# Optimization experiments

Measured on AMD Instinct MI355X. Metric: run time of the kernel, lower is better.

## Reference

```python
import jax, jax.numpy as jnp
import numpy as np

N_LAYERS = 2
D_CONV = 4
D_MODEL = 768
D_INNER = 1536
D_STATE = 16
D_DELTA = 48
B = 2
L = 1024
EPS = 1e-5


def setup_inputs() -> dict:
    key = jax.random.key(0)
    ks = jax.random.split(key, 8)
    s = 0.02
    x = jax.random.normal(ks[0], (B, L, D_MODEL), jnp.float32)
    in_proj_w = jax.random.normal(ks[1], (N_LAYERS, 2 * D_INNER, D_MODEL), jnp.float32) * s
    conv_w = jax.random.normal(ks[2], (N_LAYERS, D_INNER, 1, D_CONV), jnp.float32) * s
    conv_b = jnp.zeros((N_LAYERS, D_INNER), jnp.float32)
    xproj_w = jax.random.normal(ks[3], (N_LAYERS, D_DELTA + 2 * D_STATE, D_INNER), jnp.float32) * s
    dt_w = jax.random.normal(ks[4], (N_LAYERS, D_INNER, D_DELTA), jnp.float32) * s
    dt_b = jax.random.normal(ks[5], (N_LAYERS, D_INNER), jnp.float32) * s
    A_log = jnp.tile(jnp.log(jnp.arange(1, D_STATE + 1, dtype=jnp.float32)), (N_LAYERS, D_INNER, 1))
    D = jnp.ones((N_LAYERS, D_INNER), jnp.float32)
    out_proj_w = jax.random.normal(ks[6], (N_LAYERS, D_MODEL, D_INNER), jnp.float32) * s
    norm_w = jnp.ones((N_LAYERS, D_MODEL), jnp.float32)
    return dict(x=x, in_proj_w=in_proj_w, conv_w=conv_w, conv_b=conv_b,
                xproj_w=xproj_w, dt_w=dt_w, dt_b=dt_b, A_log=A_log, D=D,
                out_proj_w=out_proj_w, norm_w=norm_w)


def rms_norm(x, w):
    return w * x * jax.lax.rsqrt(jnp.mean(x * x, axis=-1, keepdims=True) + EPS)


def causal_depthwise_conv(x, w, b):
    # x: [B, L, D_INNER], w: [D_INNER, 1, K], b: [D_INNER]
    xc = x.transpose(0, 2, 1)  # [B, D, L]
    y = jax.lax.conv_general_dilated(
        xc, w, window_strides=(1,), padding=[(D_CONV - 1, 0)],
        dimension_numbers=("NCH", "OIH", "NCH"), feature_group_count=D_INNER)
    y = y + b[None, :, None]
    return y.transpose(0, 2, 1)  # [B, L, D]


def ssm(x, A_log, D, xproj_w, dt_w, dt_b):
    # x: [B, L, D_INNER]
    A = -jnp.exp(A_log)  # [D, N]
    dbc = jnp.einsum('bld,ed->ble', x, xproj_w)
    delta, Bc, C = jnp.split(dbc, [D_DELTA, D_DELTA + D_STATE], axis=-1)
    delta = jax.nn.softplus(jnp.einsum('blr,dr->bld', delta, dt_w) + dt_b)  # [B, L, D]
    dA = jnp.exp(delta[..., None] * A)                          # [B, L, D, N]
    dBx = delta[..., None] * Bc[:, :, None, :] * x[..., None]   # [B, L, D, N]

    def step(h, inp):
        dA_t, dBx_t, C_t = inp
        h = dA_t * h + dBx_t                      # [B, D, N]
        y = jnp.einsum('bdn,bn->bd', h, C_t)      # [B, D]
        return h, y

    h0 = jnp.zeros((x.shape[0], D_INNER, D_STATE), x.dtype)
    _, ys = jax.lax.scan(step, h0, (dA.transpose(1, 0, 2, 3),
                                    dBx.transpose(1, 0, 2, 3),
                                    C.transpose(1, 0, 2)))
    y = ys.transpose(1, 0, 2)  # [B, L, D]
    return y + D * x


def mamba_block(x, in_w, cw, cb, xp_w, dtw, dtb, Alog, Dp, out_w):
    xz = jnp.einsum('blm,em->ble', x, in_w)           # [B, L, 2*D_INNER]
    xi, z = jnp.split(xz, 2, axis=-1)
    xi = jax.nn.silu(causal_depthwise_conv(xi, cw, cb))
    y = ssm(xi, Alog, Dp, xp_w, dtw, dtb)
    out = y * jax.nn.silu(z)
    return jnp.einsum('bld,md->blm', out, out_w)


def reference(x, in_proj_w, conv_w, conv_b, xproj_w, dt_w, dt_b, A_log, D, out_proj_w, norm_w):
    for i in range(N_LAYERS):
        x = x + mamba_block(rms_norm(x, norm_w[i]), in_proj_w[i], conv_w[i], conv_b[i],
                            xproj_w[i], dt_w[i], dt_b[i], A_log[i], D[i], out_proj_w[i])
    return x
```

## Files before the change

kernel.cpp:

```cpp
#include <hip/hip_runtime.h>
#include <hip/hip_bf16.h>
#include <cstdint>

#define NL 2
#define DM 768
#define DI 1536
#define DS 16
#define DD 48
#define DCONV 4
#define BB 2
#define LL 1024
#define MROWS (BB*LL)
#define DBCW (DD + 2*DS)
#define TC 32
#define NC (LL/TC)
#define KSPL 4
#define XPN 128

typedef __bf16 bf16x8 __attribute__((ext_vector_type(8)));
typedef float f32x4 __attribute__((ext_vector_type(4)));
using bf16 = __hip_bfloat16;

__device__ __forceinline__ float softplusf(float x) {
  return (x > 20.f) ? x : log1pf(__expf(x));
}

__device__ __forceinline__ void load_lds16(const void* g, void* l) {
  __builtin_amdgcn_global_load_lds(
      (const __attribute__((address_space(1))) void*)g,
      (__attribute__((address_space(3))) void*)l, 16, 0, 0);
}

#define WI_N (NL*2*DI*DM)
#define WX_N (NL*XPN*DI)
#define WD_N (NL*DI*DD)
#define WO_N (NL*DM*DI)
__global__ __launch_bounds__(256)
void prep_weights(const float* __restrict__ wi, const float* __restrict__ wx,
                  const float* __restrict__ wd, const float* __restrict__ wo,
                  bf16* __restrict__ bi, bf16* __restrict__ bx,
                  bf16* __restrict__ bd, bf16* __restrict__ bo)
{
  int i = blockIdx.x * 256 + threadIdx.x;
  if (i < WI_N) { bi[i] = __float2bfloat16(wi[i]); return; }
  i -= WI_N;
  if (i < WX_N) {
    const int l = i / (XPN*DI), r = (i / DI) % XPN, k = i % DI;
    const float v = (r < DBCW) ? wx[((size_t)l*DBCW + r)*DI + k] : 0.f;
    bx[i] = __float2bfloat16(v); return;
  }
  i -= WX_N;
  if (i < WD_N) { bd[i] = __float2bfloat16(wd[i]); return; }
  i -= WD_N;
  if (i < WO_N) { bo[i] = __float2bfloat16(wo[i]); }
}

__global__ __launch_bounds__(256)
void rmsnorm_kernel(const float* __restrict__ x, const float* __restrict__ w,
                    bf16* __restrict__ out)
{
  const int row = blockIdx.x;
  const float* xr = x + (size_t)row * DM;
  const int t = threadIdx.x;
  float v0 = xr[t], v1 = xr[t + 256], v2 = xr[t + 512];
  float ss = v0*v0 + v1*v1 + v2*v2;
  #pragma unroll
  for (int off = 32; off > 0; off >>= 1) ss += __shfl_down(ss, off);
  __shared__ float sred[4];
  if ((t & 63) == 0) sred[t >> 6] = ss;
  __syncthreads();
  const float scale = rsqrtf((sred[0]+sred[1]+sred[2]+sred[3]) * (1.f/DM) + 1e-5f);
  out[(size_t)row*DM + t      ] = __float2bfloat16(v0 * scale * w[t]);
  out[(size_t)row*DM + t + 256] = __float2bfloat16(v1 * scale * w[t + 256]);
  out[(size_t)row*DM + t + 512] = __float2bfloat16(v2 * scale * w[t + 512]);
}

__global__ __launch_bounds__(256)
void gemm_in128(const bf16* __restrict__ A, const bf16* __restrict__ W,
                float* __restrict__ xzf, bf16* __restrict__ zb)
{
  __shared__ __align__(16) bf16 As[128][32];
  __shared__ __align__(16) bf16 Ws[128][32];
  const int tid = threadIdx.x;
  const int wave = tid >> 6, lane = tid & 63;
  const int m0 = blockIdx.x * 128, n0 = blockIdx.y * 128;
  const int wr = (wave >> 1) * 64, wc = (wave & 1) * 64;
  const int l16 = lane & 15, quad = lane >> 4;
  const int srow = wave * 16 + (lane >> 2);
  const int scol = (lane & 3) * 8;
  bf16* a_base0 = &As[wave*16][0];
  bf16* a_base1 = &As[64 + wave*16][0];
  bf16* w_base0 = &Ws[wave*16][0];
  bf16* w_base1 = &Ws[64 + wave*16][0];

  f32x4 acc[4][4] = {};

  for (int k0 = 0; k0 < DM; k0 += 32) {
    load_lds16(A + (size_t)(m0 + srow) * DM + k0 + scol,      a_base0);
    load_lds16(A + (size_t)(m0 + 64 + srow) * DM + k0 + scol, a_base1);
    load_lds16(W + (size_t)(n0 + srow) * DM + k0 + scol,      w_base0);
    load_lds16(W + (size_t)(n0 + 64 + srow) * DM + k0 + scol, w_base1);
    __syncthreads();

    bf16x8 af[4], wf[4];
    #pragma unroll
    for (int i = 0; i < 4; ++i)
      af[i] = *reinterpret_cast<const bf16x8*>(&As[wr + i*16 + l16][quad*8]);
    #pragma unroll
    for (int j = 0; j < 4; ++j)
      wf[j] = *reinterpret_cast<const bf16x8*>(&Ws[wc + j*16 + l16][quad*8]);
    #pragma unroll
    for (int i = 0; i < 4; ++i)
      #pragma unroll
      for (int j = 0; j < 4; ++j)
        acc[i][j] = __builtin_amdgcn_mfma_f32_16x16x32_bf16(af[i], wf[j], acc[i][j], 0, 0, 0);
    __syncthreads();
  }

  const bool isz = (n0 >= DI);
  #pragma unroll
  for (int i = 0; i < 4; ++i) {
    #pragma unroll
    for (int j = 0; j < 4; ++j) {
      const int col = n0 + wc + j*16 + l16;
      #pragma unroll
      for (int r = 0; r < 4; ++r) {
        const int row = m0 + wr + i*16 + quad*4 + r;
        const float v = acc[i][j][r];
        if (!isz) xzf[(size_t)row*DI + col] = v;
        else      zb[(size_t)row*DI + col - DI] = __float2bfloat16(v);
      }
    }
  }
}

template<int MODE>
__global__ __launch_bounds__(256)
void gemm64l(const bf16* __restrict__ A, int lda,
             const bf16* __restrict__ W, int ldw,
             float* __restrict__ C, int ldc, int N, int K,
             const float* __restrict__ res)
{
  __shared__ __align__(16) bf16 As[64][32];
  __shared__ __align__(16) bf16 Ws[64][32];
  const int tid = threadIdx.x;
  const int wave = tid >> 6, lane = tid & 63;
  const int m0 = blockIdx.x * 64, n0 = blockIdx.y * 64;
  const int wr = (wave >> 1) * 32, wc = (wave & 1) * 32;
  const int l16 = lane & 15, quad = lane >> 4;
  const int srow = wave * 16 + (lane >> 2);
  const int scol = (lane & 3) * 8;
  bf16* a_base = &As[wave*16][0];
  bf16* w_base = &Ws[wave*16][0];

  A += (size_t)blockIdx.z * K;
  W += (size_t)blockIdx.z * K;
  C += (size_t)blockIdx.z * MROWS * ldc;

  f32x4 acc[2][2] = {};

  for (int k0 = 0; k0 < K; k0 += 32) {
    load_lds16(A + (size_t)(m0 + srow) * lda + k0 + scol, a_base);
    load_lds16(W + (size_t)(n0 + srow) * ldw + k0 + scol, w_base);
    __syncthreads();
    bf16x8 af[2], wf[2];
    #pragma unroll
    for (int i = 0; i < 2; ++i)
      af[i] = *reinterpret_cast<const bf16x8*>(&As[wr + i*16 + l16][quad*8]);
    #pragma unroll
    for (int j = 0; j < 2; ++j)
      wf[j] = *reinterpret_cast<const bf16x8*>(&Ws[wc + j*16 + l16][quad*8]);
    #pragma unroll
    for (int i = 0; i < 2; ++i)
      #pragma unroll
      for (int j = 0; j < 2; ++j)
        acc[i][j] = __builtin_amdgcn_mfma_f32_16x16x32_bf16(af[i], wf[j], acc[i][j], 0, 0, 0);
    __syncthreads();
  }

  #pragma unroll
  for (int i = 0; i < 2; ++i) {
    #pragma unroll
    for (int j = 0; j < 2; ++j) {
      const int col = n0 + wc + j*16 + l16;
      if (col >= N) continue;
      #pragma unroll
      for (int r = 0; r < 4; ++r) {
        const int row = m0 + wr + i*16 + quad*4 + r;
        float v = acc[i][j][r];
        const size_t idx = (size_t)row * ldc + col;
        if (MODE == 3) v += res[idx];
        C[idx] = v;
      }
    }
  }
}

__global__ __launch_bounds__(256)
void xproj_reduce(const float* __restrict__ part, bf16* __restrict__ dbcb,
                  float* __restrict__ bcf)
{
  const int idx = blockIdx.x * 256 + threadIdx.x;
  const int row = idx / DBCW, col = idx % DBCW;
  float v = part[idx];
  #pragma unroll
  for (int z = 1; z < KSPL; ++z) v += part[idx + (size_t)z*MROWS*DBCW];
  if (col < DD) dbcb[(size_t)row*DD + col] = __float2bfloat16(v);
  else          bcf[(size_t)row*32 + col - DD] = v;
}

__global__ __launch_bounds__(256)
void conv_silu_kernel(const float* __restrict__ xzf, const float* __restrict__ cw,
                      const float* __restrict__ cb, bf16* __restrict__ xob)
{
  const int idx = blockIdx.x * 256 + threadIdx.x;
  const int d = idx % DI;
  const int row = idx / DI;
  const int l = row % LL;
  float acc = cb[d];
  #pragma unroll
  for (int k = 0; k < DCONV; ++k) {
    const int ll = l - (DCONV-1) + k;
    if (ll >= 0)
      acc += cw[d*DCONV + k] * xzf[(size_t)(row - (DCONV-1) + k) * DI + d];
  }
  const float s = acc / (1.f + __expf(-acc));
  xob[idx] = __float2bfloat16(s);
}

__global__ __launch_bounds__(256)
void gemm_dt(const bf16* __restrict__ A, const bf16* __restrict__ W,
             bf16* __restrict__ Cb, const float* __restrict__ bias)
{
  __shared__ __align__(16) bf16 As[64][40];
  __shared__ __align__(16) bf16 Ws[64][40];
  const int tid = threadIdx.x;
  const int m0 = blockIdx.x * 64, n0 = blockIdx.y * 64;
  const int wave = tid >> 6, lane = tid & 63;
  const int wr = (wave >> 1) * 32, wc = (wave & 1) * 32;
  const int l16 = lane & 15, quad = lane >> 4;
  const int srow = tid >> 2;
  const int scol = (tid & 3) * 8;

  f32x4 acc[2][2] = {};

  #pragma unroll
  for (int k0 = 0; k0 < DD; k0 += 32) {
    {
      const bf16* src = A + (size_t)(m0 + srow) * DD + (k0 + scol);
      bf16* dst = &As[srow][scol];
      if (k0 + scol + 8 <= DD) {
        *reinterpret_cast<uint4*>(dst) = *reinterpret_cast<const uint4*>(src);
      } else {
        #pragma unroll
        for (int j = 0; j < 8; ++j)
          dst[j] = (k0 + scol + j < DD) ? src[j] : __float2bfloat16(0.f);
      }
    }
    {
      const bf16* src = W + (size_t)(n0 + srow) * DD + (k0 + scol);
      bf16* dst = &Ws[srow][scol];
      if (k0 + scol + 8 <= DD) {
        *reinterpret_cast<uint4*>(dst) = *reinterpret_cast<const uint4*>(src);
      } else {
        #pragma unroll
        for (int j = 0; j < 8; ++j)
          dst[j] = (k0 + scol + j < DD) ? src[j] : __float2bfloat16(0.f);
      }
    }
    __syncthreads();
    bf16x8 af[2], wf[2];
    #pragma unroll
    for (int i = 0; i < 2; ++i)
      af[i] = *reinterpret_cast<const bf16x8*>(&As[wr + i*16 + l16][quad*8]);
    #pragma unroll
    for (int j = 0; j < 2; ++j)
      wf[j] = *reinterpret_cast<const bf16x8*>(&Ws[wc + j*16 + l16][quad*8]);
    #pragma unroll
    for (int i = 0; i < 2; ++i)
      #pragma unroll
      for (int j = 0; j < 2; ++j)
        acc[i][j] = __builtin_amdgcn_mfma_f32_16x16x32_bf16(af[i], wf[j], acc[i][j], 0, 0, 0);
    __syncthreads();
  }

  #pragma unroll
  for (int i = 0; i < 2; ++i) {
    #pragma unroll
    for (int j = 0; j < 2; ++j) {
      const int col = n0 + wc + j*16 + l16;
      #pragma unroll
      for (int r = 0; r < 4; ++r) {
        const int row = m0 + wr + i*16 + quad*4 + r;
        Cb[(size_t)row*DI + col] = __float2bfloat16(softplusf(acc[i][j][r] + bias[col]));
      }
    }
  }
}

__global__ __launch_bounds__(256)
void scan_pass1(const bf16* __restrict__ delta, const bf16* __restrict__ xi,
                const float* __restrict__ bcf, const float* __restrict__ A_log,
                float* __restrict__ P, float* __restrict__ H)
{
  __shared__ float Bs[TC][DS];
  const int tid = threadIdx.x;
  const int wave = tid >> 6, lane = tid & 63;
  const int s = lane >> 5;
  const int dloc = wave*32 + (lane & 31);
  const int dt = blockIdx.x % (DI/128);
  const int c  = (blockIdx.x / (DI/128)) % NC;
  const int b  =  blockIdx.x / ((DI/128)*NC);
  const int d  = dt*128 + dloc;
  const int t0 = c*TC;

  {
    const int t = tid >> 4, n = tid & 15;
    Bs[t][n]      = bcf[((size_t)b*LL + t0 + t)*32 + n];
    Bs[t + 16][n] = bcf[((size_t)b*LL + t0 + 16 + t)*32 + n];
  }
  float An[8];
  {
    const float4* ap = (const float4*)(A_log + (size_t)d*DS + s*8);
    float4 v0 = ap[0], v1 = ap[1];
    An[0] = -__expf(v0.x)*1.44269504f; An[1] = -__expf(v0.y)*1.44269504f;
    An[2] = -__expf(v0.z)*1.44269504f; An[3] = -__expf(v0.w)*1.44269504f;
    An[4] = -__expf(v1.x)*1.44269504f; An[5] = -__expf(v1.y)*1.44269504f;
    An[6] = -__expf(v1.z)*1.44269504f; An[7] = -__expf(v1.w)*1.44269504f;
  }
  __syncthreads();

  const bf16* dptr = delta + ((size_t)b*LL + t0)*DI + d;
  const bf16* xptr = xi    + ((size_t)b*LL + t0)*DI + d;
  float h[8] = {0.f,0.f,0.f,0.f,0.f,0.f,0.f,0.f};
  float sdl = 0.f;
  #pragma unroll
  for (int t = 0; t < TC; ++t) {
    const float dl = __bfloat162float(dptr[(size_t)t*DI]);
    const float xv = __bfloat162float(xptr[(size_t)t*DI]);
    const float dlxv = dl * xv;
    sdl += dl;
    const float4* brow = (const float4*)&Bs[t][s*8];
    const float4 b0 = brow[0], b1 = brow[1];
    const float bb[8] = {b0.x,b0.y,b0.z,b0.w,b1.x,b1.y,b1.z,b1.w};
    #pragma unroll
    for (int n = 0; n < 8; ++n) {
      const float dA = exp2f(dl * An[n]);
      h[n] = dA*h[n] + dlxv*bb[n];
    }
  }
  const size_t base = (((size_t)b*NC + c)*DI + d)*DS + s*8;
  float4* Pp = (float4*)(P + base);
  float4* Hp = (float4*)(H + base);
  Pp[0] = make_float4(exp2f(An[0]*sdl), exp2f(An[1]*sdl), exp2f(An[2]*sdl), exp2f(An[3]*sdl));
  Pp[1] = make_float4(exp2f(An[4]*sdl), exp2f(An[5]*sdl), exp2f(An[6]*sdl), exp2f(An[7]*sdl));
  Hp[0] = make_float4(h[0],h[1],h[2],h[3]);
  Hp[1] = make_float4(h[4],h[5],h[6],h[7]);
}

__global__ __launch_bounds__(256)
void scan_fix(const float* __restrict__ P, float* __restrict__ H)
{
  const int idx = blockIdx.x * 256 + threadIdx.x;
  const int n = idx & 15;
  const int d = (idx >> 4) % DI;
  const int b = idx / (DS * DI);
  float hin = 0.f;
  #pragma unroll 8
  for (int c = 0; c < NC; ++c) {
    const size_t ic = (((size_t)b*NC + c)*DI + d)*DS + n;
    const float Pv = P[ic];
    const float Hv = H[ic];
    H[ic] = hin;
    hin = fmaf(Pv, hin, Hv);
  }
}

__global__ __launch_bounds__(256)
void scan_pass2(const bf16* __restrict__ delta, const bf16* __restrict__ xi,
                const float* __restrict__ bcf, const float* __restrict__ A_log,
                const float* __restrict__ H, const float* __restrict__ Dp,
                const bf16* __restrict__ zb, bf16* __restrict__ outb)
{
  __shared__ float Bs[TC][DS];
  __shared__ float Cs[TC][DS];
  const int tid = threadIdx.x;
  const int wave = tid >> 6, lane = tid & 63;
  const int s = lane >> 5;
  const int dloc = wave*32 + (lane & 31);
  const int dt = blockIdx.x % (DI/128);
  const int c  = (blockIdx.x / (DI/128)) % NC;
  const int b  =  blockIdx.x / ((DI/128)*NC);
  const int d  = dt*128 + dloc;
  const int t0 = c*TC;

  {
    const int t = tid >> 4, n = tid & 15;
    const size_t r0 = ((size_t)b*LL + t0 + t)*32;
    const size_t r1 = ((size_t)b*LL + t0 + 16 + t)*32;
    Bs[t][n]      = bcf[r0 + n];
    Bs[t + 16][n] = bcf[r1 + n];
    Cs[t][n]      = bcf[r0 + 16 + n];
    Cs[t + 16][n] = bcf[r1 + 16 + n];
  }
  float An[8];
  {
    const float4* ap = (const float4*)(A_log + (size_t)d*DS + s*8);
    float4 v0 = ap[0], v1 = ap[1];
    An[0] = -__expf(v0.x)*1.44269504f; An[1] = -__expf(v0.y)*1.44269504f;
    An[2] = -__expf(v0.z)*1.44269504f; An[3] = -__expf(v0.w)*1.44269504f;
    An[4] = -__expf(v1.x)*1.44269504f; An[5] = -__expf(v1.y)*1.44269504f;
    An[6] = -__expf(v1.z)*1.44269504f; An[7] = -__expf(v1.w)*1.44269504f;
  }
  const float Dd = Dp[d];
  float h[8];
  {
    const float4* hp = (const float4*)(H + (((size_t)b*NC + c)*DI + d)*DS + s*8);
    float4 h0 = hp[0], h1 = hp[1];
    h[0]=h0.x; h[1]=h0.y; h[2]=h0.z; h[3]=h0.w;
    h[4]=h1.x; h[5]=h1.y; h[6]=h1.z; h[7]=h1.w;
  }
  __syncthreads();

  const bf16* dptr = delta + ((size_t)b*LL + t0)*DI + d;
  const bf16* xptr = xi    + ((size_t)b*LL + t0)*DI + d;
  const bf16* zptr = zb    + ((size_t)b*LL + t0)*DI + d;
  bf16* optr = outb + ((size_t)b*LL + t0)*DI + d;

  #pragma unroll
  for (int t = 0; t < TC; ++t) {
    const float dl = __bfloat162float(dptr[(size_t)t*DI]);
    const float xv = __bfloat162float(xptr[(size_t)t*DI]);
    const float zv = __bfloat162float(zptr[(size_t)t*DI]);
    const float dlxv = dl * xv;
    const float4* brow = (const float4*)&Bs[t][s*8];
    const float4* crow = (const float4*)&Cs[t][s*8];
    const float4 b0 = brow[0], b1 = brow[1];
    const float4 c0 = crow[0], c1 = crow[1];
    const float bb[8] = {b0.x,b0.y,b0.z,b0.w,b1.x,b1.y,b1.z,b1.w};
    const float cc[8] = {c0.x,c0.y,c0.z,c0.w,c1.x,c1.y,c1.z,c1.w};
    float y = 0.f;
    #pragma unroll
    for (int n = 0; n < 8; ++n) {
      const float dA = exp2f(dl * An[n]);
      h[n] = dA*h[n] + dlxv*bb[n];
      y = fmaf(h[n], cc[n], y);
    }
    y += __shfl_xor(y, 32);
    if (s == 0) {
      const float o = (y + Dd * xv) * (zv / (1.f + __expf(-zv)));
      optr[(size_t)t*DI] = __float2bfloat16(o);
    }
  }
}

extern "C" void kernel_launch(void* const* d_in, const int* in_sizes, int n_in,
                              void* d_out, int out_size, void* d_ws, size_t ws_size,
                              hipStream_t stream)
{
  const float* x_in   = (const float*)d_in[0];
  const float* w_inp  = (const float*)d_in[1];
  const float* w_conv = (const float*)d_in[2];
  const float* b_conv = (const float*)d_in[3];
  const float* w_xprj = (const float*)d_in[4];
  const float* w_dtp  = (const float*)d_in[5];
  const float* b_dt   = (const float*)d_in[6];
  const float* a_log  = (const float*)d_in[7];
  const float* d_par  = (const float*)d_in[8];
  const float* w_outp = (const float*)d_in[9];
  const float* w_norm = (const float*)d_in[10];
  float* xfinal = (float*)d_out;

  char* ws = (char*)d_ws;
  size_t off = 0;
  auto alloc = [&](size_t bytes) -> void* {
    void* p = ws + off;
    off += (bytes + 255) & ~(size_t)255;
    return p;
  };
  bf16*  wb_in  = (bf16*) alloc((size_t)WI_N*2);
  bf16*  wb_xp  = (bf16*) alloc((size_t)WX_N*2);
  bf16*  wb_dt  = (bf16*) alloc((size_t)WD_N*2);
  bf16*  wb_out = (bf16*) alloc((size_t)WO_N*2);
  bf16*  xn     = (bf16*) alloc((size_t)MROWS*DM*2);
  float* xzf    = (float*)alloc((size_t)MROWS*DI*4);
  bf16*  zb     = (bf16*) alloc((size_t)MROWS*DI*2);
  bf16*  xcb    = (bf16*) alloc((size_t)MROWS*DI*2);
  float* xpart  = (float*)alloc((size_t)KSPL*MROWS*DBCW*4);
  bf16*  dbcb   = (bf16*) alloc((size_t)MROWS*DD*2);
  float* bcf    = (float*)alloc((size_t)MROWS*32*4);
  bf16*  dltb   = (bf16*) alloc((size_t)MROWS*DI*2);
  bf16*  scb    = (bf16*) alloc((size_t)MROWS*DI*2);
  float* x1     = (float*)alloc((size_t)MROWS*DM*4);
  float* Pws    = (float*)alloc((size_t)BB*NC*DI*DS*4);
  float* Hws    = (float*)alloc((size_t)BB*NC*DI*DS*4);

  prep_weights<<<(WI_N+WX_N+WD_N+WO_N + 255)/256, 256, 0, stream>>>(
      w_inp, w_xprj, w_dtp, w_outp, wb_in, wb_xp, wb_dt, wb_out);

  const float* xprev = x_in;
  for (int l = 0; l < NL; ++l) {
    rmsnorm_kernel<<<MROWS, 256, 0, stream>>>(xprev, w_norm + l*DM, xn);

    gemm_in128<<<dim3(MROWS/128, (2*DI)/128), 256, 0, stream>>>(
        xn, wb_in + (size_t)l*2*DI*DM, xzf, zb);

    conv_silu_kernel<<<(MROWS*DI)/256, 256, 0, stream>>>(
        xzf, w_conv + l*DI*DCONV, b_conv + l*DI, xcb);

    gemm64l<0><<<dim3(MROWS/64, XPN/64, KSPL), 256, 0, stream>>>(
        xcb, DI, wb_xp + (size_t)l*XPN*DI, DI, xpart, DBCW, DBCW, DI/KSPL, nullptr);

    xproj_reduce<<<(MROWS*DBCW)/256, 256, 0, stream>>>(xpart, dbcb, bcf);

    gemm_dt<<<dim3(MROWS/64, DI/64), 256, 0, stream>>>(
        dbcb, wb_dt + (size_t)l*DI*DD, dltb, b_dt + l*DI);

    scan_pass1<<<BB*NC*(DI/128), 256, 0, stream>>>(
        dltb, xcb, bcf, a_log + (size_t)l*DI*DS, Pws, Hws);
    scan_fix<<<(BB*DI*DS)/256, 256, 0, stream>>>(Pws, Hws);
    scan_pass2<<<BB*NC*(DI/128), 256, 0, stream>>>(
        dltb, xcb, bcf, a_log + (size_t)l*DI*DS, Hws, d_par + l*DI, zb, scb);

    float* xout = (l == NL-1) ? xfinal : x1;
    gemm64l<3><<<dim3(MROWS/64, DM/64, 1), 256, 0, stream>>>(
        scb, DI, wb_out + (size_t)l*DM*DI, DI, xout, DM, DM, DI, xprev);

    xprev = x1;
  }
}
```

Before: 392.4 us.

## Fuse x-proj split-K reduce and dt projection into scan passes; store x in bf16

Removes the xproj_reduce and gemm_dt kernels. Each scan pass block now sums the split-K partials for its 32-timestep chunk, runs the small dt GEMM with MFMA into shared memory, and applies softplus before the recurrence. This cuts two launches and the global round trips for the delta, B and C buffers. The in-projection x half is also stored as bf16 instead of fp32, which halves the conv input traffic at some precision cost. In exchange, delta is computed twice (once in each pass) and the dt weights are reloaded for every chunk block.

```diff
diff --git a/kernel.cpp b/kernel.cpp
--- a/kernel.cpp
+++ b/kernel.cpp
@@ -13,7 +13,7 @@
 #define MROWS (BB*LL)
 #define DBCW (DD + 2*DS)
 #define TC 32
-#define NC (LL/TC)
+#define NCH (LL/TC)
 #define KSPL 4
 #define XPN 128
 
@@ -77,7 +77,7 @@
 
 __global__ __launch_bounds__(256)
 void gemm_in128(const bf16* __restrict__ A, const bf16* __restrict__ W,
-                float* __restrict__ xzf, bf16* __restrict__ zb)
+                bf16* __restrict__ xb, bf16* __restrict__ zb)
 {
   __shared__ __align__(16) bf16 As[128][32];
   __shared__ __align__(16) bf16 Ws[128][32];
@@ -127,7 +127,7 @@
       for (int r = 0; r < 4; ++r) {
         const int row = m0 + wr + i*16 + quad*4 + r;
         const float v = acc[i][j][r];
-        if (!isz) xzf[(size_t)row*DI + col] = v;
+        if (!isz) xb[(size_t)row*DI + col]      = __float2bfloat16(v);
         else      zb[(size_t)row*DI + col - DI] = __float2bfloat16(v);
       }
     }
@@ -197,20 +197,7 @@
 }
 
 __global__ __launch_bounds__(256)
-void xproj_reduce(const float* __restrict__ part, bf16* __restrict__ dbcb,
-                  float* __restrict__ bcf)
-{
-  const int idx = blockIdx.x * 256 + threadIdx.x;
-  const int row = idx / DBCW, col = idx % DBCW;
-  float v = part[idx];
-  #pragma unroll
-  for (int z = 1; z < KSPL; ++z) v += part[idx + (size_t)z*MROWS*DBCW];
-  if (col < DD) dbcb[(size_t)row*DD + col] = __float2bfloat16(v);
-  else          bcf[(size_t)row*32 + col - DD] = v;
-}
-
-__global__ __launch_bounds__(256)
-void conv_silu_kernel(const float* __restrict__ xzf, const float* __restrict__ cw,
+void conv_silu_kernel(const bf16* __restrict__ xb, const float* __restrict__ cw,
                       const float* __restrict__ cb, bf16* __restrict__ xob)
 {
   const int idx = blockIdx.x * 256 + threadIdx.x;
@@ -222,103 +209,95 @@
   for (int k = 0; k < DCONV; ++k) {
     const int ll = l - (DCONV-1) + k;
     if (ll >= 0)
-      acc += cw[d*DCONV + k] * xzf[(size_t)(row - (DCONV-1) + k) * DI + d];
+      acc += cw[d*DCONV + k] * __bfloat162float(xb[(size_t)(row - (DCONV-1) + k) * DI + d]);
   }
   const float s = acc / (1.f + __expf(-acc));
   xob[idx] = __float2bfloat16(s);
 }
 
-__global__ __launch_bounds__(256)
-void gemm_dt(const bf16* __restrict__ A, const bf16* __restrict__ W,
-             bf16* __restrict__ Cb, const float* __restrict__ bias)
-{
-  __shared__ __align__(16) bf16 As[64][40];
-  __shared__ __align__(16) bf16 Ws[64][40];
+template<bool WANT_C>
+__device__ __forceinline__ void stage_and_delta(
+    const float* __restrict__ xpart, const bf16* __restrict__ wdt,
+    const float* __restrict__ biasp, int b, int t0, int d0,
+    bf16 (*Adt)[64], bf16 (*Wdt)[64], float (*Ds)[128],
+    float (*Bsp)[DS], float (*Csp)[DS])
+{
   const int tid = threadIdx.x;
-  const int m0 = blockIdx.x * 64, n0 = blockIdx.y * 64;
-  const int wave = tid >> 6, lane = tid & 63;
-  const int wr = (wave >> 1) * 32, wc = (wave & 1) * 32;
+  constexpr int NCOLS = WANT_C ? DBCW : (DD + DS);
+  for (int idx = tid; idx < 32*NCOLS; idx += 256) {
+    const int t = idx / NCOLS, col = idx % NCOLS;
+    const size_t rbase = ((size_t)b*LL + t0 + t)*DBCW + col;
+    float v = xpart[rbase];
+    #pragma unroll
+    for (int z = 1; z < KSPL; ++z) v += xpart[rbase + (size_t)z*(MROWS*DBCW)];
+    if (col < DD)            Adt[t][col] = __float2bfloat16(v);
+    else if (col < DD + DS)  Bsp[t][col - DD] = v;
+    else if (WANT_C)         Csp[t][col - DD - DS] = v;
+  }
+  if (tid < 64) {
+    *reinterpret_cast<uint4*>(&Adt[tid >> 1][48 + (tid & 1)*8]) = make_uint4(0,0,0,0);
+  }
+  for (int idx = tid; idx < 128*6; idx += 256) {
+    const int r = idx / 6, c8 = (idx % 6) * 8;
+    *reinterpret_cast<uint4*>(&Wdt[r][c8]) =
+        *reinterpret_cast<const uint4*>(wdt + (size_t)(d0 + r)*DD + c8);
+  }
+  *reinterpret_cast<uint4*>(&Wdt[tid >> 1][48 + (tid & 1)*8]) = make_uint4(0,0,0,0);
+  __syncthreads();
+
+  const int wv = tid >> 6, lane = tid & 63;
   const int l16 = lane & 15, quad = lane >> 4;
-  const int srow = tid >> 2;
-  const int scol = (tid & 3) * 8;
-
-  f32x4 acc[2][2] = {};
-
-  #pragma unroll
-  for (int k0 = 0; k0 < DD; k0 += 32) {
-    {
-      const bf16* src = A + (size_t)(m0 + srow) * DD + (k0 + scol);
-      bf16* dst = &As[srow][scol];
-      if (k0 + scol + 8 <= DD) {
-        *reinterpret_cast<uint4*>(dst) = *reinterpret_cast<const uint4*>(src);
-      } else {
-        #pragma unroll
-        for (int j = 0; j < 8; ++j)
-          dst[j] = (k0 + scol + j < DD) ? src[j] : __float2bfloat16(0.f);
-      }
-    }
-    {
-      const bf16* src = W + (size_t)(n0 + srow) * DD + (k0 + scol);
-      bf16* dst = &Ws[srow][scol];
-      if (k0 + scol + 8 <= DD) {
-        *reinterpret_cast<uint4*>(dst) = *reinterpret_cast<const uint4*>(src);
-      } else {
-        #pragma unroll
-        for (int j = 0; j < 8; ++j)
-          dst[j] = (k0 + scol + j < DD) ? src[j] : __float2bfloat16(0.f);
-      }
-    }
-    __syncthreads();
+  f32x4 dacc[2][2] = {};
+  #pragma unroll
+  for (int kk = 0; kk < 2; ++kk) {
     bf16x8 af[2], wf[2];
     #pragma unroll
     for (int i = 0; i < 2; ++i)
-      af[i] = *reinterpret_cast<const bf16x8*>(&As[wr + i*16 + l16][quad*8]);
+      af[i] = *reinterpret_cast<const bf16x8*>(&Adt[i*16 + l16][kk*32 + quad*8]);
     #pragma unroll
     for (int j = 0; j < 2; ++j)
-      wf[j] = *reinterpret_cast<const bf16x8*>(&Ws[wc + j*16 + l16][quad*8]);
+      wf[j] = *reinterpret_cast<const bf16x8*>(&Wdt[wv*32 + j*16 + l16][kk*32 + quad*8]);
     #pragma unroll
     for (int i = 0; i < 2; ++i)
       #pragma unroll
       for (int j = 0; j < 2; ++j)
-        acc[i][j] = __builtin_amdgcn_mfma_f32_16x16x32_bf16(af[i], wf[j], acc[i][j], 0, 0, 0);
-    __syncthreads();
-  }
-
+        dacc[i][j] = __builtin_amdgcn_mfma_f32_16x16x32_bf16(af[i], wf[j], dacc[i][j], 0, 0, 0);
+  }
   #pragma unroll
   for (int i = 0; i < 2; ++i) {
     #pragma unroll
     for (int j = 0; j < 2; ++j) {
-      const int col = n0 + wc + j*16 + l16;
+      const int col = wv*32 + j*16 + l16;
+      const float bias = biasp[col];
       #pragma unroll
-      for (int r = 0; r < 4; ++r) {
-        const int row = m0 + wr + i*16 + quad*4 + r;
-        Cb[(size_t)row*DI + col] = __float2bfloat16(softplusf(acc[i][j][r] + bias[col]));
-      }
+      for (int r = 0; r < 4; ++r)
+        Ds[i*16 + quad*4 + r][col] = softplusf(dacc[i][j][r] + bias);
     }
   }
-}
-
-__global__ __launch_bounds__(256)
-void scan_pass1(const bf16* __restrict__ delta, const bf16* __restrict__ xi,
-                const float* __restrict__ bcf, const float* __restrict__ A_log,
+  __syncthreads();
+}
+
+__global__ __launch_bounds__(256)
+void scan_pass1(const float* __restrict__ xpart, const bf16* __restrict__ xi,
+                const bf16* __restrict__ wdt, const float* __restrict__ dtb,
+                const float* __restrict__ A_log,
                 float* __restrict__ P, float* __restrict__ H)
 {
+  __shared__ __align__(16) bf16 Adt[32][64];
+  __shared__ __align__(16) bf16 Wdt[128][64];
+  __shared__ float Ds[32][128];
   __shared__ float Bs[TC][DS];
   const int tid = threadIdx.x;
   const int wave = tid >> 6, lane = tid & 63;
   const int s = lane >> 5;
   const int dloc = wave*32 + (lane & 31);
   const int dt = blockIdx.x % (DI/128);
-  const int c  = (blockIdx.x / (DI/128)) % NC;
-  const int b  =  blockIdx.x / ((DI/128)*NC);
-  const int d  = dt*128 + dloc;
+  const int c  = (blockIdx.x / (DI/128)) % NCH;
+  const int b  =  blockIdx.x / ((DI/128)*NCH);
+  const int d0 = dt*128;
+  const int d  = d0 + dloc;
   const int t0 = c*TC;
 
-  {
-    const int t = tid >> 4, n = tid & 15;
-    Bs[t][n]      = bcf[((size_t)b*LL + t0 + t)*32 + n];
-    Bs[t + 16][n] = bcf[((size_t)b*LL + t0 + 16 + t)*32 + n];
-  }
   float An[8];
   {
     const float4* ap = (const float4*)(A_log + (size_t)d*DS + s*8);
@@ -328,15 +307,16 @@
     An[4] = -__expf(v1.x)*1.44269504f; An[5] = -__expf(v1.y)*1.44269504f;
     An[6] = -__expf(v1.z)*1.44269504f; An[7] = -__expf(v1.w)*1.44269504f;
   }
-  __syncthreads();
-
-  const bf16* dptr = delta + ((size_t)b*LL + t0)*DI + d;
-  const bf16* xptr = xi    + ((size_t)b*LL + t0)*DI + d;
+
+  stage_and_delta<false>(xpart, wdt, dtb + d0, b, t0, d0, Adt, Wdt, Ds, Bs,
+                         (float(*)[DS])nullptr);
+
+  const bf16* xptr = xi + ((size_t)b*LL + t0)*DI + d;
   float h[8] = {0.f,0.f,0.f,0.f,0.f,0.f,0.f,0.f};
   float sdl = 0.f;
   #pragma unroll
   for (int t = 0; t < TC; ++t) {
-    const float dl = __bfloat162float(dptr[(size_t)t*DI]);
+    const float dl = Ds[t][dloc];
     const float xv = __bfloat162float(xptr[(size_t)t*DI]);
     const float dlxv = dl * xv;
     sdl += dl;
@@ -349,7 +329,7 @@
       h[n] = dA*h[n] + dlxv*bb[n];
     }
   }
-  const size_t base = (((size_t)b*NC + c)*DI + d)*DS + s*8;
+  const size_t base = (((size_t)b*NCH + c)*DI + d)*DS + s*8;
   float4* Pp = (float4*)(P + base);
   float4* Hp = (float4*)(H + base);
   Pp[0] = make_float4(exp2f(An[0]*sdl), exp2f(An[1]*sdl), exp2f(An[2]*sdl), exp2f(An[3]*sdl));
@@ -367,8 +347,8 @@
   const int b = idx / (DS * DI);
   float hin = 0.f;
   #pragma unroll 8
-  for (int c = 0; c < NC; ++c) {
-    const size_t ic = (((size_t)b*NC + c)*DI + d)*DS + n;
+  for (int c = 0; c < NCH; ++c) {
+    const size_t ic = (((size_t)b*NCH + c)*DI + d)*DS + n;
     const float Pv = P[ic];
     const float Hv = H[ic];
     H[ic] = hin;
@@ -377,11 +357,15 @@
 }
 
 __global__ __launch_bounds__(256)
-void scan_pass2(const bf16* __restrict__ delta, const bf16* __restrict__ xi,
-                const float* __restrict__ bcf, const float* __restrict__ A_log,
+void scan_pass2(const float* __restrict__ xpart, const bf16* __restrict__ xi,
+                const bf16* __restrict__ wdt, const float* __restrict__ dtb,
+                const float* __restrict__ A_log,
                 const float* __restrict__ H, const float* __restrict__ Dp,
                 const bf16* __restrict__ zb, bf16* __restrict__ outb)
 {
+  __shared__ __align__(16) bf16 Adt[32][64];
+  __shared__ __align__(16) bf16 Wdt[128][64];
+  __shared__ float Ds[32][128];
   __shared__ float Bs[TC][DS];
   __shared__ float Cs[TC][DS];
   const int tid = threadIdx.x;
@@ -389,20 +373,12 @@
   const int s = lane >> 5;
   const int dloc = wave*32 + (lane & 31);
   const int dt = blockIdx.x % (DI/128);
-  const int c  = (blockIdx.x / (DI/128)) % NC;
-  const int b  =  blockIdx.x / ((DI/128)*NC);
-  const int d  = dt*128 + dloc;
+  const int c  = (blockIdx.x / (DI/128)) % NCH;
+  const int b  =  blockIdx.x / ((DI/128)*NCH);
+  const int d0 = dt*128;
+  const int d  = d0 + dloc;
   const int t0 = c*TC;
 
-  {
-    const int t = tid >> 4, n = tid & 15;
-    const size_t r0 = ((size_t)b*LL + t0 + t)*32;
-    const size_t r1 = ((size_t)b*LL + t0 + 16 + t)*32;
-    Bs[t][n]      = bcf[r0 + n];
-    Bs[t + 16][n] = bcf[r1 + n];
-    Cs[t][n]      = bcf[r0 + 16 + n];
-    Cs[t + 16][n] = bcf[r1 + 16 + n];
-  }
   float An[8];
   {
     const float4* ap = (const float4*)(A_log + (size_t)d*DS + s*8);
@@ -415,21 +391,21 @@
   const float Dd = Dp[d];
   float h[8];
   {
-    const float4* hp = (const float4*)(H + (((size_t)b*NC + c)*DI + d)*DS + s*8);
+    const float4* hp = (const float4*)(H + (((size_t)b*NCH + c)*DI + d)*DS + s*8);
     float4 h0 = hp[0], h1 = hp[1];
     h[0]=h0.x; h[1]=h0.y; h[2]=h0.z; h[3]=h0.w;
     h[4]=h1.x; h[5]=h1.y; h[6]=h1.z; h[7]=h1.w;
   }
-  __syncthreads();
-
-  const bf16* dptr = delta + ((size_t)b*LL + t0)*DI + d;
-  const bf16* xptr = xi    + ((size_t)b*LL + t0)*DI + d;
-  const bf16* zptr = zb    + ((size_t)b*LL + t0)*DI + d;
+
+  stage_and_delta<true>(xpart, wdt, dtb + d0, b, t0, d0, Adt, Wdt, Ds, Bs, Cs);
+
+  const bf16* xptr = xi + ((size_t)b*LL + t0)*DI + d;
+  const bf16* zptr = zb + ((size_t)b*LL + t0)*DI + d;
   bf16* optr = outb + ((size_t)b*LL + t0)*DI + d;
 
   #pragma unroll
   for (int t = 0; t < TC; ++t) {
-    const float dl = __bfloat162float(dptr[(size_t)t*DI]);
+    const float dl = Ds[t][dloc];
     const float xv = __bfloat162float(xptr[(size_t)t*DI]);
     const float zv = __bfloat162float(zptr[(size_t)t*DI]);
     const float dlxv = dl * xv;
@@ -483,17 +459,14 @@
   bf16*  wb_dt  = (bf16*) alloc((size_t)WD_N*2);
   bf16*  wb_out = (bf16*) alloc((size_t)WO_N*2);
   bf16*  xn     = (bf16*) alloc((size_t)MROWS*DM*2);
-  float* xzf    = (float*)alloc((size_t)MROWS*DI*4);
+  bf16*  xb     = (bf16*) alloc((size_t)MROWS*DI*2);
   bf16*  zb     = (bf16*) alloc((size_t)MROWS*DI*2);
   bf16*  xcb    = (bf16*) alloc((size_t)MROWS*DI*2);
   float* xpart  = (float*)alloc((size_t)KSPL*MROWS*DBCW*4);
-  bf16*  dbcb   = (bf16*) alloc((size_t)MROWS*DD*2);
-  float* bcf    = (float*)alloc((size_t)MROWS*32*4);
-  bf16*  dltb   = (bf16*) alloc((size_t)MROWS*DI*2);
   bf16*  scb    = (bf16*) alloc((size_t)MROWS*DI*2);
   float* x1     = (float*)alloc((size_t)MROWS*DM*4);
-  float* Pws    = (float*)alloc((size_t)BB*NC*DI*DS*4);
-  float* Hws    = (float*)alloc((size_t)BB*NC*DI*DS*4);
+  float* Pws    = (float*)alloc((size_t)BB*NCH*DI*DS*4);
+  float* Hws    = (float*)alloc((size_t)BB*NCH*DI*DS*4);
 
   prep_weights<<<(WI_N+WX_N+WD_N+WO_N + 255)/256, 256, 0, stream>>>(
       w_inp, w_xprj, w_dtp, w_outp, wb_in, wb_xp, wb_dt, wb_out);
@@ -503,24 +476,21 @@
     rmsnorm_kernel<<<MROWS, 256, 0, stream>>>(xprev, w_norm + l*DM, xn);
 
     gemm_in128<<<dim3(MROWS/128, (2*DI)/128), 256, 0, stream>>>(
-        xn, wb_in + (size_t)l*2*DI*DM, xzf, zb);
+        xn, wb_in + (size_t)l*2*DI*DM, xb, zb);
 
     conv_silu_kernel<<<(MROWS*DI)/256, 256, 0, stream>>>(
-        xzf, w_conv + l*DI*DCONV, b_conv + l*DI, xcb);
+        xb, w_conv + l*DI*DCONV, b_conv + l*DI, xcb);
 
     gemm64l<0><<<dim3(MROWS/64, XPN/64, KSPL), 256, 0, stream>>>(
         xcb, DI, wb_xp + (size_t)l*XPN*DI, DI, xpart, DBCW, DBCW, DI/KSPL, nullptr);
 
-    xproj_reduce<<<(MROWS*DBCW)/256, 256, 0, stream>>>(xpart, dbcb, bcf);
-
-    gemm_dt<<<dim3(MROWS/64, DI/64), 256, 0, stream>>>(
-        dbcb, wb_dt + (size_t)l*DI*DD, dltb, b_dt + l*DI);
-
-    scan_pass1<<<BB*NC*(DI/128), 256, 0, stream>>>(
-        dltb, xcb, bcf, a_log + (size_t)l*DI*DS, Pws, Hws);
+    scan_pass1<<<BB*NCH*(DI/128), 256, 0, stream>>>(
+        xpart, xcb, wb_dt + (size_t)l*DI*DD, b_dt + l*DI,
+        a_log + (size_t)l*DI*DS, Pws, Hws);
     scan_fix<<<(BB*DI*DS)/256, 256, 0, stream>>>(Pws, Hws);
-    scan_pass2<<<BB*NC*(DI/128), 256, 0, stream>>>(
-        dltb, xcb, bcf, a_log + (size_t)l*DI*DS, Hws, d_par + l*DI, zb, scb);
+    scan_pass2<<<BB*NCH*(DI/128), 256, 0, stream>>>(
+        xpart, xcb, wb_dt + (size_t)l*DI*DD, b_dt + l*DI,
+        a_log + (size_t)l*DI*DS, Hws, d_par + l*DI, zb, scb);
 
     float* xout = (l == NL-1) ? xfinal : x1;
     gemm64l<3><<<dim3(MROWS/64, DM/64, 1), 256, 0, stream>>>(
```

Result: no change. 399.9 us (+1.9%).

## Store x branch as bf16, halve scan chunk size, prefetch scan inputs

Applied to the files above, without the earlier changes.

The in-projection GEMM now writes the x half in bf16 instead of fp32, and the conv kernel reads bf16, which halves that intermediate's traffic. The scan chunk length drops from 32 to 16, doubling the number of blocks for parallelism but also doubling the chunk-state workspace and the serial length of scan_fix. Both scan passes now load all delta, x and z values for the chunk into registers up front so the loads are issued together before the recurrence. The bf16 rounding of x before the conv adds some precision loss.

```diff
diff --git a/kernel.cpp b/kernel.cpp
--- a/kernel.cpp
+++ b/kernel.cpp
@@ -12,8 +12,8 @@
 #define LL 1024
 #define MROWS (BB*LL)
 #define DBCW (DD + 2*DS)
-#define TC 32
-#define NC (LL/TC)
+#define TC 16
+#define NCH (LL/TC)
 #define KSPL 4
 #define XPN 128
 
@@ -23,6 +23,10 @@
 
 __device__ __forceinline__ float softplusf(float x) {
   return (x > 20.f) ? x : log1pf(__expf(x));
+}
+
+__device__ __forceinline__ float bfu2f(ushort u) {
+  return __uint_as_float((uint32_t)u << 16);
 }
 
 __device__ __forceinline__ void load_lds16(const void* g, void* l) {
@@ -77,7 +81,7 @@
 
 __global__ __launch_bounds__(256)
 void gemm_in128(const bf16* __restrict__ A, const bf16* __restrict__ W,
-                float* __restrict__ xzf, bf16* __restrict__ zb)
+                bf16* __restrict__ xb, bf16* __restrict__ zb)
 {
   __shared__ __align__(16) bf16 As[128][32];
   __shared__ __align__(16) bf16 Ws[128][32];
@@ -127,7 +131,7 @@
       for (int r = 0; r < 4; ++r) {
         const int row = m0 + wr + i*16 + quad*4 + r;
         const float v = acc[i][j][r];
-        if (!isz) xzf[(size_t)row*DI + col] = v;
+        if (!isz) xb[(size_t)row*DI + col]      = __float2bfloat16(v);
         else      zb[(size_t)row*DI + col - DI] = __float2bfloat16(v);
       }
     }
@@ -210,7 +214,7 @@
 }
 
 __global__ __launch_bounds__(256)
-void conv_silu_kernel(const float* __restrict__ xzf, const float* __restrict__ cw,
+void conv_silu_kernel(const bf16* __restrict__ xb, const float* __restrict__ cw,
                       const float* __restrict__ cb, bf16* __restrict__ xob)
 {
   const int idx = blockIdx.x * 256 + threadIdx.x;
@@ -222,7 +226,7 @@
   for (int k = 0; k < DCONV; ++k) {
     const int ll = l - (DCONV-1) + k;
     if (ll >= 0)
-      acc += cw[d*DCONV + k] * xzf[(size_t)(row - (DCONV-1) + k) * DI + d];
+      acc += cw[d*DCONV + k] * __bfloat162float(xb[(size_t)(row - (DCONV-1) + k) * DI + d]);
   }
   const float s = acc / (1.f + __expf(-acc));
   xob[idx] = __float2bfloat16(s);
@@ -309,16 +313,24 @@
   const int s = lane >> 5;
   const int dloc = wave*32 + (lane & 31);
   const int dt = blockIdx.x % (DI/128);
-  const int c  = (blockIdx.x / (DI/128)) % NC;
-  const int b  =  blockIdx.x / ((DI/128)*NC);
+  const int c  = (blockIdx.x / (DI/128)) % NCH;
+  const int b  =  blockIdx.x / ((DI/128)*NCH);
   const int d  = dt*128 + dloc;
   const int t0 = c*TC;
 
   {
     const int t = tid >> 4, n = tid & 15;
-    Bs[t][n]      = bcf[((size_t)b*LL + t0 + t)*32 + n];
-    Bs[t + 16][n] = bcf[((size_t)b*LL + t0 + 16 + t)*32 + n];
-  }
+    Bs[t][n] = bcf[((size_t)b*LL + t0 + t)*32 + n];
+  }
+
+  const ushort* dptr = (const ushort*)(delta + ((size_t)b*LL + t0)*DI + d);
+  const ushort* xptr = (const ushort*)(xi    + ((size_t)b*LL + t0)*DI + d);
+  ushort dls[TC], xvs[TC];
+  #pragma unroll
+  for (int t = 0; t < TC; ++t) dls[t] = dptr[(size_t)t*DI];
+  #pragma unroll
+  for (int t = 0; t < TC; ++t) xvs[t] = xptr[(size_t)t*DI];
+
   float An[8];
   {
     const float4* ap = (const float4*)(A_log + (size_t)d*DS + s*8);
@@ -330,14 +342,12 @@
   }
   __syncthreads();
 
-  const bf16* dptr = delta + ((size_t)b*LL + t0)*DI + d;
-  const bf16* xptr = xi    + ((size_t)b*LL + t0)*DI + d;
   float h[8] = {0.f,0.f,0.f,0.f,0.f,0.f,0.f,0.f};
   float sdl = 0.f;
   #pragma unroll
   for (int t = 0; t < TC; ++t) {
-    const float dl = __bfloat162float(dptr[(size_t)t*DI]);
-    const float xv = __bfloat162float(xptr[(size_t)t*DI]);
+    const float dl = bfu2f(dls[t]);
+    const float xv = bfu2f(xvs[t]);
     const float dlxv = dl * xv;
     sdl += dl;
     const float4* brow = (const float4*)&Bs[t][s*8];
@@ -349,7 +359,7 @@
       h[n] = dA*h[n] + dlxv*bb[n];
     }
   }
-  const size_t base = (((size_t)b*NC + c)*DI + d)*DS + s*8;
+  const size_t base = (((size_t)b*NCH + c)*DI + d)*DS + s*8;
   float4* Pp = (float4*)(P + base);
   float4* Hp = (float4*)(H + base);
   Pp[0] = make_float4(exp2f(An[0]*sdl), exp2f(An[1]*sdl), exp2f(An[2]*sdl), exp2f(An[3]*sdl));
@@ -367,8 +377,8 @@
   const int b = idx / (DS * DI);
   float hin = 0.f;
   #pragma unroll 8
-  for (int c = 0; c < NC; ++c) {
-    const size_t ic = (((size_t)b*NC + c)*DI + d)*DS + n;
+  for (int c = 0; c < NCH; ++c) {
+    const size_t ic = (((size_t)b*NCH + c)*DI + d)*DS + n;
     const float Pv = P[ic];
     const float Hv = H[ic];
     H[ic] = hin;
@@ -389,20 +399,29 @@
   const int s = lane >> 5;
   const int dloc = wave*32 + (lane & 31);
   const int dt = blockIdx.x % (DI/128);
-  const int c  = (blockIdx.x / (DI/128)) % NC;
-  const int b  =  blockIdx.x / ((DI/128)*NC);
+  const int c  = (blockIdx.x / (DI/128)) % NCH;
+  const int b  =  blockIdx.x / ((DI/128)*NCH);
   const int d  = dt*128 + dloc;
   const int t0 = c*TC;
 
   {
     const int t = tid >> 4, n = tid & 15;
     const size_t r0 = ((size_t)b*LL + t0 + t)*32;
-    const size_t r1 = ((size_t)b*LL + t0 + 16 + t)*32;
-    Bs[t][n]      = bcf[r0 + n];
-    Bs[t + 16][n] = bcf[r1 + n];
-    Cs[t][n]      = bcf[r0 + 16 + n];
-    Cs[t + 16][n] = bcf[r1 + 16 + n];
-  }
+    Bs[t][n] = bcf[r0 + n];
+    Cs[t][n] = bcf[r0 + 16 + n];
+  }
+
+  const ushort* dptr = (const ushort*)(delta + ((size_t)b*LL + t0)*DI + d);
+  const ushort* xptr = (const ushort*)(xi    + ((size_t)b*LL + t0)*DI + d);
+  const ushort* zptr = (const ushort*)(zb    + ((size_t)b*LL + t0)*DI + d);
+  ushort dls[TC], xvs[TC], zvs[TC];
+  #pragma unroll
+  for (int t = 0; t < TC; ++t) dls[t] = dptr[(size_t)t*DI];
+  #pragma unroll
+  for (int t = 0; t < TC; ++t) xvs[t] = xptr[(size_t)t*DI];
+  #pragma unroll
+  for (int t = 0; t < TC; ++t) zvs[t] = zptr[(size_t)t*DI];
+
   float An[8];
   {
     const float4* ap = (const float4*)(A_log + (size_t)d*DS + s*8);
@@ -415,23 +434,20 @@
   const float Dd = Dp[d];
   float h[8];
   {
-    const float4* hp = (const float4*)(H + (((size_t)b*NC + c)*DI + d)*DS + s*8);
+    const float4* hp = (const float4*)(H + (((size_t)b*NCH + c)*DI + d)*DS + s*8);
     float4 h0 = hp[0], h1 = hp[1];
     h[0]=h0.x; h[1]=h0.y; h[2]=h0.z; h[3]=h0.w;
     h[4]=h1.x; h[5]=h1.y; h[6]=h1.z; h[7]=h1.w;
   }
   __syncthreads();
 
-  const bf16* dptr = delta + ((size_t)b*LL + t0)*DI + d;
-  const bf16* xptr = xi    + ((size_t)b*LL + t0)*DI + d;
-  const bf16* zptr = zb    + ((size_t)b*LL + t0)*DI + d;
   bf16* optr = outb + ((size_t)b*LL + t0)*DI + d;
 
   #pragma unroll
   for (int t = 0; t < TC; ++t) {
-    const float dl = __bfloat162float(dptr[(size_t)t*DI]);
-    const float xv = __bfloat162float(xptr[(size_t)t*DI]);
-    const float zv = __bfloat162float(zptr[(size_t)t*DI]);
+    const float dl = bfu2f(dls[t]);
+    const float xv = bfu2f(xvs[t]);
+    const float zv = bfu2f(zvs[t]);
     const float dlxv = dl * xv;
     const float4* brow = (const float4*)&Bs[t][s*8];
     const float4* crow = (const float4*)&Cs[t][s*8];
@@ -483,7 +499,7 @@
   bf16*  wb_dt  = (bf16*) alloc((size_t)WD_N*2);
   bf16*  wb_out = (bf16*) alloc((size_t)WO_N*2);
   bf16*  xn     = (bf16*) alloc((size_t)MROWS*DM*2);
-  float* xzf    = (float*)alloc((size_t)MROWS*DI*4);
+  bf16*  xb     = (bf16*) alloc((size_t)MROWS*DI*2);
   bf16*  zb     = (bf16*) alloc((size_t)MROWS*DI*2);
   bf16*  xcb    = (bf16*) alloc((size_t)MROWS*DI*2);
   float* xpart  = (float*)alloc((size_t)KSPL*MROWS*DBCW*4);
@@ -492,8 +508,8 @@
   bf16*  dltb   = (bf16*) alloc((size_t)MROWS*DI*2);
   bf16*  scb    = (bf16*) alloc((size_t)MROWS*DI*2);
   float* x1     = (float*)alloc((size_t)MROWS*DM*4);
-  float* Pws    = (float*)alloc((size_t)BB*NC*DI*DS*4);
-  float* Hws    = (float*)alloc((size_t)BB*NC*DI*DS*4);
+  float* Pws    = (float*)alloc((size_t)BB*NCH*DI*DS*4);
+  float* Hws    = (float*)alloc((size_t)BB*NCH*DI*DS*4);
 
   prep_weights<<<(WI_N+WX_N+WD_N+WO_N + 255)/256, 256, 0, stream>>>(
       w_inp, w_xprj, w_dtp, w_outp, wb_in, wb_xp, wb_dt, wb_out);
@@ -503,10 +519,10 @@
     rmsnorm_kernel<<<MROWS, 256, 0, stream>>>(xprev, w_norm + l*DM, xn);
 
     gemm_in128<<<dim3(MROWS/128, (2*DI)/128), 256, 0, stream>>>(
-        xn, wb_in + (size_t)l*2*DI*DM, xzf, zb);
+        xn, wb_in + (size_t)l*2*DI*DM, xb, zb);
 
     conv_silu_kernel<<<(MROWS*DI)/256, 256, 0, stream>>>(
-        xzf, w_conv + l*DI*DCONV, b_conv + l*DI, xcb);
+        xb, w_conv + l*DI*DCONV, b_conv + l*DI, xcb);
 
     gemm64l<0><<<dim3(MROWS/64, XPN/64, KSPL), 256, 0, stream>>>(
         xcb, DI, wb_xp + (size_t)l*XPN*DI, DI, xpart, DBCW, DBCW, DI/KSPL, nullptr);
@@ -516,10 +532,10 @@
     gemm_dt<<<dim3(MROWS/64, DI/64), 256, 0, stream>>>(
         dbcb, wb_dt + (size_t)l*DI*DD, dltb, b_dt + l*DI);
 
-    scan_pass1<<<BB*NC*(DI/128), 256, 0, stream>>>(
+    scan_pass1<<<BB*NCH*(DI/128), 256, 0, stream>>>(
         dltb, xcb, bcf, a_log + (size_t)l*DI*DS, Pws, Hws);
     scan_fix<<<(BB*DI*DS)/256, 256, 0, stream>>>(Pws, Hws);
-    scan_pass2<<<BB*NC*(DI/128), 256, 0, stream>>>(
+    scan_pass2<<<BB*NCH*(DI/128), 256, 0, stream>>>(
         dltb, xcb, bcf, a_log + (size_t)l*DI*DS, Hws, d_par + l*DI, zb, scb);
 
     float* xout = (l == NL-1) ? xfinal : x1;
```

After: 364.5 us. 1.08x faster.
